# Kernel optimization log

Measured on AMD Instinct MI355X. Metric: run time of the kernel, lower is better.

The kernel has to match this reference:

```python
import jax, jax.numpy as jnp
import numpy as np

NUM_USERS = 100000
NUM_POIS = 50000
DIM = 128
NUM_EDGES = 3_200_000


def setup_inputs() -> dict:
    key = jax.random.key(0)
    ks = jax.random.split(key, 8)
    return {
        "user_idx": jax.random.randint(ks[0], (1,), 0, NUM_USERS, dtype=jnp.int64 if jax.config.jax_enable_x64 else jnp.int32).astype(jnp.int32),
        "poi_embeddings": jax.random.normal(ks[1], (NUM_POIS, DIM), dtype=jnp.float32),
        "edge_src": jax.random.randint(ks[2], (NUM_EDGES,), 0, NUM_USERS, dtype=jnp.int32),
        "edge_dst": jax.random.randint(ks[3], (NUM_EDGES,), 0, NUM_POIS, dtype=jnp.int32),
        "edge_freq": jax.random.randint(ks[4], (NUM_EDGES,), 1, 50, dtype=jnp.int32),
        "user_emb": jax.random.normal(ks[5], (NUM_USERS, DIM), dtype=jnp.float32),
        "fc_w": jax.random.normal(ks[6], (DIM, 2 * DIM), dtype=jnp.float32) * (1.0 / np.sqrt(2 * DIM)),
        "fc_b": jax.random.normal(ks[7], (DIM,), dtype=jnp.float32) * 0.01,
    }


def reference(user_idx, poi_embeddings, edge_src, edge_dst, edge_freq, user_emb, fc_w, fc_b):
    # user embedding lookup: [1, d]
    u = user_emb[user_idx]
    # mask edges belonging to this user, weights = visit frequencies
    mask = edge_src == user_idx[0]
    w = jnp.where(mask, edge_freq.astype(jnp.float32), 0.0)  # [E]
    # scatter masked frequencies onto POI ids, then one [P] x [P,d] contraction
    # == sum over matched edges of freq * poi_embeddings[dst]
    acc = jnp.zeros((poi_embeddings.shape[0],), poi_embeddings.dtype).at[edge_dst].add(w)
    num = acc @ poi_embeddings  # [d]
    denom = w.sum()
    safe = jnp.where(denom > 0, denom, 1.0)
    neigh = jnp.where(denom > 0, num / safe, 0.0)[None, :]  # [1, d]; zeros if no edges
    combined = jnp.concatenate([u, neigh], axis=1)  # [1, 2d]
    return combined @ fc_w.T + fc_b
```

## Files before the change

### kernel.cpp

```cpp
#include <hip/hip_runtime.h>

#define DIM 128


__global__ void scan_accum_kernel(const int* __restrict__ user_idx,
                                  const int* __restrict__ edge_src,
                                  const int* __restrict__ edge_dst,
                                  const int* __restrict__ edge_freq,
                                  int E,
                                  const float* __restrict__ poi,
                                  float* __restrict__ num,
                                  float* __restrict__ den) {
    const int uid = user_idx[0];
    const int lane = threadIdx.x & 63;
    const int gtid = blockIdx.x * blockDim.x + threadIdx.x;
    const int stride = gridDim.x * blockDim.x;
    const int E4 = E >> 2;
    const int4* __restrict__ src4 = (const int4*)edge_src;

    for (int i4 = gtid; i4 < E4; i4 += stride) {
        const int4 s = src4[i4];
        const bool any = (s.x == uid) | (s.y == uid) | (s.z == uid) | (s.w == uid);
        if (__any(any)) {
            const int base = i4 * 4;
            const int sv[4] = {s.x, s.y, s.z, s.w};
#pragma unroll
            for (int j = 0; j < 4; ++j) {
                const bool m = (sv[j] == uid);
                int dst = 0, f = 0;
                if (m) { dst = edge_dst[base + j]; f = edge_freq[base + j]; }
                unsigned long long b = __ballot(m);
                while (b) {
                    const int sl = (int)__ffsll(b) - 1;
                    b &= b - 1;
                    const int   ddst = __shfl(dst, sl);
                    const float fv   = (float)__shfl(f, sl);
                    const float* row = poi + (size_t)ddst * DIM;
                    const float v0 = row[lane];
                    const float v1 = row[lane + 64];
                    atomicAdd(&num[lane],      fv * v0);
                    atomicAdd(&num[lane + 64], fv * v1);
                    if (lane == 0) atomicAdd(den, fv);
                }
            }
        }
    }
    for (int i = E4 * 4 + gtid; i < E; i += stride) {
        if (edge_src[i] == uid) {
            const float fv = (float)edge_freq[i];
            const float* row = poi + (size_t)edge_dst[i] * DIM;
            for (int k = 0; k < DIM; ++k) atomicAdd(&num[k], fv * row[k]);
            atomicAdd(den, fv);
        }
    }
}

__global__ void __launch_bounds__(DIM)
finish_kernel(const int* __restrict__ user_idx,
              const float* __restrict__ user_emb,
              const float* __restrict__ fc_w,
              const float* __restrict__ fc_b,
              const float* __restrict__ num,
              const float* __restrict__ den,
              float* __restrict__ out) {
    __shared__ float comb[2 * DIM];
    const int d = threadIdx.x;

    const float dv = *den;
    const float neigh = (dv > 0.0f) ? (num[d] / dv) : 0.0f;

    const int uid = user_idx[0];
    comb[d]       = user_emb[(size_t)uid * DIM + d];
    comb[DIM + d] = neigh;
    __syncthreads();

    const float4* __restrict__ w4 = (const float4*)(fc_w + (size_t)d * (2 * DIM));
    float acc = fc_b[d];
#pragma unroll 8
    for (int k = 0; k < (2 * DIM) / 4; ++k) {
        const float4 w = w4[k];
        acc += w.x * comb[4 * k + 0] + w.y * comb[4 * k + 1] +
               w.z * comb[4 * k + 2] + w.w * comb[4 * k + 3];
    }
    out[d] = acc;
}

extern "C" void kernel_launch(void* const* d_in, const int* in_sizes, int n_in,
                              void* d_out, int out_size, void* d_ws, size_t ws_size,
                              hipStream_t stream) {
    const int*   user_idx  = (const int*)d_in[0];
    const float* poi       = (const float*)d_in[1];
    const int*   edge_src  = (const int*)d_in[2];
    const int*   edge_dst  = (const int*)d_in[3];
    const int*   edge_freq = (const int*)d_in[4];
    const float* user_emb  = (const float*)d_in[5];
    const float* fc_w      = (const float*)d_in[6];
    const float* fc_b      = (const float*)d_in[7];
    float* out = (float*)d_out;

    const int E = in_sizes[2];

    char* ws = (char*)d_ws;
    float* num = (float*)ws;
    float* den = (float*)(ws + 512);

    hipMemsetAsync(ws, 0, 640, stream);

    const int threads = 256;
    const int E4 = E >> 2;
    int blocks = (E4 + threads - 1) / threads;
    if (blocks < 1) blocks = 1;
    if (blocks > 65535) blocks = 65535;

    scan_accum_kernel<<<blocks, threads, 0, stream>>>(
        user_idx, edge_src, edge_dst, edge_freq, E, poi, num, den);

    finish_kernel<<<1, DIM, 0, stream>>>(
        user_idx, user_emb, fc_w, fc_b, num, den, out);
}
```

Baseline: 132.9 us.

## Replace global atomics with per-block partials and parallel finish reduction

Each block now keeps per-wave register accumulators for the matched edges and writes one partial row per block to the workspace. This removes the global atomics and the memset launch. The scan is capped at 1024 blocks, each loading four int4 source chunks per iteration. The finish kernel grows to 1024 threads, which reduce the partials and split the FC matvec across 8 groups. The cost is a serial two-stage reduction, and the scan may stream edge_src with lower occupancy.

```diff
diff --git a/kernel.cpp b/kernel.cpp
--- a/kernel.cpp
+++ b/kernel.cpp
@@ -1,88 +1,177 @@
 #include <hip/hip_runtime.h>
 
 #define DIM 128
-
-
-__global__ void scan_accum_kernel(const int* __restrict__ user_idx,
-                                  const int* __restrict__ edge_src,
-                                  const int* __restrict__ edge_dst,
-                                  const int* __restrict__ edge_freq,
-                                  int E,
-                                  const float* __restrict__ poi,
-                                  float* __restrict__ num,
-                                  float* __restrict__ den) {
-    const int uid = user_idx[0];
+#define PART_STRIDE 132
+#define SCAN_THREADS 256
+#define MAX_BLOCKS 1024
+#define FIN_THREADS 1024
+
+
+__global__ void __launch_bounds__(SCAN_THREADS)
+scan_partial_kernel(const int* __restrict__ user_idx,
+                    const int* __restrict__ edge_src,
+                    const int* __restrict__ edge_dst,
+                    const int* __restrict__ edge_freq,
+                    int E,
+                    const float* __restrict__ poi,
+                    float* __restrict__ part) {
+    const int uid  = user_idx[0];
     const int lane = threadIdx.x & 63;
+    const int wv   = threadIdx.x >> 6;
     const int gtid = blockIdx.x * blockDim.x + threadIdx.x;
-    const int stride = gridDim.x * blockDim.x;
+    const int total = gridDim.x * blockDim.x;
     const int E4 = E >> 2;
     const int4* __restrict__ src4 = (const int4*)edge_src;
 
-    for (int i4 = gtid; i4 < E4; i4 += stride) {
-        const int4 s = src4[i4];
-        const bool any = (s.x == uid) | (s.y == uid) | (s.z == uid) | (s.w == uid);
+    float acc0 = 0.0f, acc1 = 0.0f, dacc = 0.0f;
+
+    for (int base = 0; base < E4; base += 4 * total) {
+        int4 v[4];
+        int  idx[4];
+#pragma unroll
+        for (int j = 0; j < 4; ++j) {
+            idx[j] = base + gtid + j * total;
+            v[j] = (idx[j] < E4) ? src4[idx[j]] : make_int4(-1, -1, -1, -1);
+        }
+        bool any = false;
+#pragma unroll
+        for (int j = 0; j < 4; ++j)
+            any |= (v[j].x == uid) | (v[j].y == uid) | (v[j].z == uid) | (v[j].w == uid);
+
         if (__any(any)) {
-            const int base = i4 * 4;
-            const int sv[4] = {s.x, s.y, s.z, s.w};
 #pragma unroll
             for (int j = 0; j < 4; ++j) {
-                const bool m = (sv[j] == uid);
-                int dst = 0, f = 0;
-                if (m) { dst = edge_dst[base + j]; f = edge_freq[base + j]; }
-                unsigned long long b = __ballot(m);
-                while (b) {
-                    const int sl = (int)__ffsll(b) - 1;
-                    b &= b - 1;
-                    const int   ddst = __shfl(dst, sl);
-                    const float fv   = (float)__shfl(f, sl);
-                    const float* row = poi + (size_t)ddst * DIM;
-                    const float v0 = row[lane];
-                    const float v1 = row[lane + 64];
-                    atomicAdd(&num[lane],      fv * v0);
-                    atomicAdd(&num[lane + 64], fv * v1);
-                    if (lane == 0) atomicAdd(den, fv);
+                const int sv[4] = {v[j].x, v[j].y, v[j].z, v[j].w};
+#pragma unroll
+                for (int c = 0; c < 4; ++c) {
+                    const bool m = (sv[c] == uid);
+                    unsigned long long b = __ballot(m);
+                    if (!b) continue;
+                    int dst = 0, f = 0;
+                    if (m) {
+                        dst = edge_dst[idx[j] * 4 + c];
+                        f   = edge_freq[idx[j] * 4 + c];
+                    }
+                    while (b) {
+                        const int sl = (int)__ffsll(b) - 1;
+                        b &= b - 1;
+                        const int   ddst = __shfl(dst, sl);
+                        const float fv   = (float)__shfl(f, sl);
+                        const float* row = poi + (size_t)ddst * DIM;
+                        acc0 += fv * row[lane];
+                        acc1 += fv * row[lane + 64];
+                        if (lane == 0) dacc += fv;
+                    }
                 }
             }
         }
     }
-    for (int i = E4 * 4 + gtid; i < E; i += stride) {
-        if (edge_src[i] == uid) {
-            const float fv = (float)edge_freq[i];
-            const float* row = poi + (size_t)edge_dst[i] * DIM;
-            for (int k = 0; k < DIM; ++k) atomicAdd(&num[k], fv * row[k]);
-            atomicAdd(den, fv);
+
+    {
+        const int i = (E4 << 2) + gtid;
+        const bool in = (i < E);
+        const int sv = in ? edge_src[i] : -1;
+        const bool m = (sv == uid);
+        unsigned long long b = __ballot(m);
+        if (b) {
+            int dst = 0, f = 0;
+            if (m) { dst = edge_dst[i]; f = edge_freq[i]; }
+            while (b) {
+                const int sl = (int)__ffsll(b) - 1;
+                b &= b - 1;
+                const int   ddst = __shfl(dst, sl);
+                const float fv   = (float)__shfl(f, sl);
+                const float* row = poi + (size_t)ddst * DIM;
+                acc0 += fv * row[lane];
+                acc1 += fv * row[lane + 64];
+                if (lane == 0) dacc += fv;
+            }
         }
     }
+
+    __shared__ float s_num[4][DIM];
+    __shared__ float s_den[4];
+    s_num[wv][lane]      = acc0;
+    s_num[wv][lane + 64] = acc1;
+    if (lane == 0) s_den[wv] = dacc;
+    __syncthreads();
+
+    float* __restrict__ row = part + (size_t)blockIdx.x * PART_STRIDE;
+    const int t = threadIdx.x;
+    if (t < DIM) {
+        row[t] = s_num[0][t] + s_num[1][t] + s_num[2][t] + s_num[3][t];
+    } else if (t == DIM) {
+        row[DIM] = s_den[0] + s_den[1] + s_den[2] + s_den[3];
+    }
 }
 
-__global__ void __launch_bounds__(DIM)
+__global__ void __launch_bounds__(FIN_THREADS)
 finish_kernel(const int* __restrict__ user_idx,
               const float* __restrict__ user_emb,
               const float* __restrict__ fc_w,
               const float* __restrict__ fc_b,
-              const float* __restrict__ num,
-              const float* __restrict__ den,
+              const float* __restrict__ part,
+              int NB,
               float* __restrict__ out) {
+    __shared__ float s_red[8][DIM];
+    __shared__ float s_wden[FIN_THREADS / 64];
+    __shared__ float s_dtot;
     __shared__ float comb[2 * DIM];
-    const int d = threadIdx.x;
-
-    const float dv = *den;
-    const float neigh = (dv > 0.0f) ? (num[d] / dv) : 0.0f;
-
-    const int uid = user_idx[0];
-    comb[d]       = user_emb[(size_t)uid * DIM + d];
-    comb[DIM + d] = neigh;
-    __syncthreads();
-
-    const float4* __restrict__ w4 = (const float4*)(fc_w + (size_t)d * (2 * DIM));
-    float acc = fc_b[d];
-#pragma unroll 8
-    for (int k = 0; k < (2 * DIM) / 4; ++k) {
+    __shared__ float s_fc[8][DIM];
+
+    const int t = threadIdx.x;
+    const int d = t & (DIM - 1);
+    const int g = t >> 7;
+
+    float s = 0.0f;
+    for (int b = g; b < NB; b += 8)
+        s += part[(size_t)b * PART_STRIDE + d];
+    s_red[g][d] = s;
+
+    float dn = 0.0f;
+    for (int b = t; b < NB; b += FIN_THREADS)
+        dn += part[(size_t)b * PART_STRIDE + DIM];
+#pragma unroll
+    for (int off = 32; off; off >>= 1) dn += __shfl_xor(dn, off);
+    if ((t & 63) == 0) s_wden[t >> 6] = dn;
+    __syncthreads();
+    if (t == 0) {
+        float v = 0.0f;
+#pragma unroll
+        for (int w = 0; w < FIN_THREADS / 64; ++w) v += s_wden[w];
+        s_dtot = v;
+    }
+    __syncthreads();
+
+    if (t < DIM) {
+        float num = 0.0f;
+#pragma unroll
+        for (int gg = 0; gg < 8; ++gg) num += s_red[gg][d];
+        const float dv = s_dtot;
+        comb[t]       = user_emb[(size_t)user_idx[0] * DIM + t];
+        comb[DIM + t] = (dv > 0.0f) ? (num / dv) : 0.0f;
+    }
+    __syncthreads();
+
+    const float4* __restrict__ w4 =
+        (const float4*)(fc_w + (size_t)d * (2 * DIM) + g * 32);
+    float acc = 0.0f;
+#pragma unroll
+    for (int k = 0; k < 8; ++k) {
         const float4 w = w4[k];
-        acc += w.x * comb[4 * k + 0] + w.y * comb[4 * k + 1] +
-               w.z * comb[4 * k + 2] + w.w * comb[4 * k + 3];
-    }
-    out[d] = acc;
+        const int kk = g * 32 + 4 * k;
+        acc += w.x * comb[kk + 0] + w.y * comb[kk + 1] +
+               w.z * comb[kk + 2] + w.w * comb[kk + 3];
+    }
+    s_fc[g][d] = acc;
+    __syncthreads();
+
+    if (t < DIM) {
+        float o = fc_b[t];
+#pragma unroll
+        for (int gg = 0; gg < 8; ++gg) o += s_fc[gg][t];
+        out[t] = o;
+    }
 }
 
 extern "C" void kernel_launch(void* const* d_in, const int* in_sizes, int n_in,
@@ -98,23 +187,20 @@
     const float* fc_b      = (const float*)d_in[7];
     float* out = (float*)d_out;
 
-    const int E = in_sizes[2];
-
-    char* ws = (char*)d_ws;
-    float* num = (float*)ws;
-    float* den = (float*)(ws + 512);
-
-    hipMemsetAsync(ws, 0, 640, stream);
-
-    const int threads = 256;
+    const int E  = in_sizes[2];
     const int E4 = E >> 2;
-    int blocks = (E4 + threads - 1) / threads;
-    if (blocks < 1) blocks = 1;
-    if (blocks > 65535) blocks = 65535;
-
-    scan_accum_kernel<<<blocks, threads, 0, stream>>>(
-        user_idx, edge_src, edge_dst, edge_freq, E, poi, num, den);
-
-    finish_kernel<<<1, DIM, 0, stream>>>(
-        user_idx, user_emb, fc_w, fc_b, num, den, out);
+    float* part = (float*)d_ws;
+
+    int NB = (E4 + 4 * SCAN_THREADS - 1) / (4 * SCAN_THREADS);
+    if (NB < 1) NB = 1;
+    NB = (NB + 7) & ~7;
+    if (NB > MAX_BLOCKS) NB = MAX_BLOCKS;
+    const int nb_cap = (int)(ws_size / (PART_STRIDE * sizeof(float)));
+    if (NB > nb_cap) NB = nb_cap;
+
+    scan_partial_kernel<<<NB, SCAN_THREADS, 0, stream>>>(
+        user_idx, edge_src, edge_dst, edge_freq, E, poi, part);
+
+    finish_kernel<<<1, FIN_THREADS, 0, stream>>>(
+        user_idx, user_emb, fc_w, fc_b, part, NB, out);
 }
```

Result: slower. 157.7 us (+18.7%).
